# Optimization experiments

Measured on AMD Instinct MI355X. Metric: run time of the kernel, lower is better.

The kernel has to match this reference:

```python
import jax, jax.numpy as jnp
import numpy as np

B, T, D = 2, 2048, 1024
H = 16
HD = D // H  # 64


def _rope_tables(t_len, hd, dtype=jnp.float32):
    inv_freq = 1.0 / (10000.0 ** (jnp.arange(0, hd, 2, dtype=jnp.float32) / hd))
    freqs = jnp.outer(jnp.arange(t_len, dtype=jnp.float32), inv_freq)  # [T, hd/2]
    emb = jnp.concatenate([freqs, freqs], axis=-1)  # [T, hd]
    return emb.astype(dtype)


def _rotate_half(x):
    x1, x2 = jnp.split(x, 2, axis=-1)
    return jnp.concatenate([-x2, x1], axis=-1)


def setup_inputs() -> dict:
    key = jax.random.key(0)
    k1, k2, k3 = jax.random.split(key, 3)
    x = jax.random.normal(k1, (B, T, D), dtype=jnp.float32)
    w_qkv = jax.random.normal(k2, (D, 3 * D), dtype=jnp.float32) * (D ** -0.5)
    w_out = jax.random.normal(k3, (D, D), dtype=jnp.float32) * (D ** -0.5)
    return {"x": x, "w_qkv": w_qkv, "w_out": w_out}


def reference(x, w_qkv, w_out):
    Bc, Tc, Dc = x.shape
    scale = HD ** -0.5
    qkv = x @ w_qkv  # [B,T,3D]
    q, k, v = jnp.split(qkv, 3, axis=-1)
    # -> [B,H,T,hd]
    q = q.reshape(Bc, Tc, H, HD).transpose(0, 2, 1, 3)
    k = k.reshape(Bc, Tc, H, HD).transpose(0, 2, 1, 3)
    v = v.reshape(Bc, Tc, H, HD).transpose(0, 2, 1, 3)
    emb = _rope_tables(Tc, HD, x.dtype)  # [T,hd]
    cos = jnp.cos(emb)[None, None, :, :]
    sin = jnp.sin(emb)[None, None, :, :]
    q = q * cos + _rotate_half(q) * sin
    k = k * cos + _rotate_half(k) * sin
    attn = jnp.einsum('bhqd,bhkd->bhqk', q, k) * scale  # [B,H,T,T]
    causal = jnp.tril(jnp.ones((Tc, Tc), dtype=bool))
    attn = jnp.where(causal[None, None], attn, -jnp.inf)
    attn = jax.nn.softmax(attn, axis=-1)
    out = jnp.einsum('bhqk,bhkd->bhqd', attn, v)
    out = out.transpose(0, 2, 1, 3).reshape(Bc, Tc, Dc)
    return out @ w_out
```

## Files before the change

kernel.cpp:

```cpp
#include <hip/hip_runtime.h>

#define TSEQ 2048
#define DMODEL 1024
#define NHEAD 16
#define HDIM 64
#define NB 2
#define MROWS 4096
#define NQKV 3072
#define QSCALE 0.1803368801111204f
#define ROPE_C (13.2877123795494f / 32.0f)
#define NEGINF -3.0e38f

using s16x8 = __attribute__((ext_vector_type(8))) short;
using s16x4 = __attribute__((ext_vector_type(4))) short;
using f32x4 = __attribute__((ext_vector_type(4))) float;
using u32x2 = __attribute__((ext_vector_type(2))) unsigned int;

static __device__ __forceinline__ float b2f(unsigned short u) {
  union { unsigned int i; float f; } x; x.i = ((unsigned int)u) << 16; return x.f;
}
static __device__ __forceinline__ unsigned short f2b(float f) {
  unsigned int u = __float_as_uint(f);
  u += 0x7fffu + ((u >> 16) & 1u);
  return (unsigned short)(u >> 16);
}

typedef const __attribute__((address_space(1))) char gchar;
typedef __attribute__((address_space(3))) char lchar;
static __device__ __forceinline__ void gload_lds16(const void* g, void* l) {
  __builtin_amdgcn_global_load_lds((gchar*)g, (lchar*)l, 16, 0, 0);
}

__global__ __launch_bounds__(256) void k_prep(const float* __restrict__ x,
                                              short* __restrict__ xb,
                                              const float* __restrict__ wq,
                                              short* __restrict__ wqT,
                                              const float* __restrict__ wo,
                                              short* __restrict__ woT) {
  __shared__ float tile[32][33];
  const int blk = blockIdx.x;
  const int tid = threadIdx.x;
  if (blk < 4096) {
    const int i = blk * 256 + tid;
    const float4 v = ((const float4*)x)[i];
    s16x4 o;
    o.x = (short)f2b(v.x); o.y = (short)f2b(v.y);
    o.z = (short)f2b(v.z); o.w = (short)f2b(v.w);
    ((s16x4*)xb)[i] = o;
    return;
  }
  const float* in; short* out; int C, bx, by;
  if (blk < 7168) {
    const int l = blk - 4096; in = wq; out = wqT; C = NQKV;
    bx = l % 96; by = l / 96;
  } else {
    const int l = blk - 7168; in = wo; out = woT; C = DMODEL;
    bx = l & 31; by = l >> 5;
  }
  const int tx = tid & 31, ty4 = (tid >> 5) * 4;
#pragma unroll
  for (int i = 0; i < 4; ++i)
    tile[ty4 + i][tx] = in[(by * 32 + ty4 + i) * C + bx * 32 + tx];
  __syncthreads();
#pragma unroll
  for (int i = 0; i < 4; ++i)
    out[(bx * 32 + ty4 + i) * DMODEL + by * 32 + tx] = (short)f2b(tile[tx][ty4 + i]);
}

__global__ __launch_bounds__(256) void k_gemm_qkv(const short* __restrict__ A,
                                                  const short* __restrict__ BT,
                                                  short* __restrict__ Qo,
                                                  short* __restrict__ Ko,
                                                  short* __restrict__ Vt) {
  __shared__ __attribute__((aligned(16))) short As[128 * 64];
  __shared__ __attribute__((aligned(16))) short Bs[128 * 64];
  const int K = DMODEL;
  const int tid = threadIdx.x;
  const int wave = tid >> 6, lane = tid & 63, quad = lane >> 4, l15 = lane & 15;
  const int wm = (wave >> 1) * 64, wn = (wave & 1) * 64;
  const int m0 = blockIdx.y * 128, n0 = blockIdx.x * 128;
  f32x4 acc[4][4] = {};
  const char* Ab = (const char*)A;
  const char* Bb = (const char*)BT;
  char* AsB = (char*)As;
  char* BsB = (char*)Bs;
  int srow[4], sg[4];
#pragma unroll
  for (int p = 0; p < 4; ++p) {
    const int i = p * 256 + tid;
    srow[p] = i >> 3;
    sg[p] = (i & 7) ^ (srow[p] & 7);
  }
  for (int k0 = 0; k0 < K; k0 += 64) {
    __syncthreads();
#pragma unroll
    for (int p = 0; p < 4; ++p) {
      const long go = ((long)(m0 + srow[p]) * K + k0) * 2 + sg[p] * 16;
      gload_lds16(Ab + go, AsB + p * 4096 + wave * 1024);
    }
#pragma unroll
    for (int p = 0; p < 4; ++p) {
      const long go = ((long)(n0 + srow[p]) * K + k0) * 2 + sg[p] * 16;
      gload_lds16(Bb + go, BsB + p * 4096 + wave * 1024);
    }
    __syncthreads();
#pragma unroll
    for (int hf = 0; hf < 2; ++hf) {
      s16x8 af[4], bf[4];
#pragma unroll
      for (int i = 0; i < 4; ++i) {
        const int ra = wm + i * 16 + l15;
        af[i] = *(const s16x8*)(AsB + ra * 128 + (((hf * 4 + quad) ^ (ra & 7)) * 16));
        const int rb = wn + i * 16 + l15;
        bf[i] = *(const s16x8*)(BsB + rb * 128 + (((hf * 4 + quad) ^ (rb & 7)) * 16));
      }
#pragma unroll
      for (int i = 0; i < 4; ++i)
#pragma unroll
        for (int j = 0; j < 4; ++j)
          acc[i][j] = __builtin_amdgcn_mfma_f32_16x16x32_bf16(af[i], bf[j], acc[i][j], 0, 0, 0);
    }
  }
  const int colbase = n0 + wn;
  const int region = colbase >> 10;
  const int hh = (colbase & 1023) >> 6;
  const int bq = m0 >> 11;
  const int tbase = (m0 & 2047) + wm;
  if (region == 2) {
    short* dst = Vt + (((long)(bq * NHEAD + hh) * HDIM) << 11);
#pragma unroll
    for (int i = 0; i < 4; ++i) {
      const int t0 = tbase + i * 16 + quad * 4;
#pragma unroll
      for (int j = 0; j < 4; ++j) {
        const int d = j * 16 + l15;
        s16x4 w;
        w.x = (short)f2b(acc[i][j][0]);
        w.y = (short)f2b(acc[i][j][1]);
        w.z = (short)f2b(acc[i][j][2]);
        w.w = (short)f2b(acc[i][j][3]);
        *(s16x4*)(dst + (((long)d) << 11) + t0) = w;
      }
    }
  } else {
    short* dst = (region ? Ko : Qo) + (long)(bq * NHEAD + hh) * TSEQ * HDIM;
#pragma unroll
    for (int i = 0; i < 4; ++i)
#pragma unroll
      for (int j = 0; j < 4; ++j) {
        const int d = j * 16 + l15;
#pragma unroll
        for (int r = 0; r < 4; ++r) {
          const int t = tbase + i * 16 + quad * 4 + r;
          dst[(long)t * HDIM + d] = (short)f2b(acc[i][j][r]);
        }
      }
  }
}

__global__ __launch_bounds__(256) void k_ropek(short* __restrict__ Kp) {
  const int tt = blockIdx.x, bh = blockIdx.y;
  const int tid = threadIdx.x;
  const int row = tid >> 2, chunk = tid & 3;
  const int t = tt * 64 + row;
  short* base = Kp + ((long)bh * TSEQ + t) * HDIM + chunk * 8;
  const s16x8 lo = *(const s16x8*)base;
  const s16x8 hi = *(const s16x8*)(base + 32);
  s16x8 nlo, nhi;
  const float tf = (float)t;
#pragma unroll
  for (int j = 0; j < 8; ++j) {
    const float inv = exp2f(-(float)(chunk * 8 + j) * ROPE_C);
    float sn, cs;
    __sincosf(tf * inv, &sn, &cs);
    const float a = b2f((unsigned short)lo[j]);
    const float b = b2f((unsigned short)hi[j]);
    nlo[j] = (short)f2b(a * cs - b * sn);
    nhi[j] = (short)f2b(b * cs + a * sn);
  }
  *(s16x8*)base = nlo;
  *(s16x8*)(base + 32) = nhi;
}

template <int IM, bool OUT_BF16>
__global__ __launch_bounds__(256) void k_gemm(const short* __restrict__ A,
                                              const short* __restrict__ BT,
                                              void* __restrict__ Cv,
                                              int M, int N, int K) {
  __shared__ __attribute__((aligned(16))) short As[IM * 32 * 64];
  __shared__ __attribute__((aligned(16))) short Bs[128 * 64];
  const int tid = threadIdx.x;
  const int wave = tid >> 6, lane = tid & 63, quad = lane >> 4, l15 = lane & 15;
  const int wm = (wave >> 1) * (IM * 16), wn = (wave & 1) * 64;
  const int m0 = blockIdx.y * (IM * 32), n0 = blockIdx.x * 128;
  f32x4 acc[IM][4] = {};
  const char* Ab = (const char*)A;
  const char* Bb = (const char*)BT;
  char* AsB = (char*)As;
  char* BsB = (char*)Bs;
  int srow[4], sg[4];
#pragma unroll
  for (int p = 0; p < 4; ++p) {
    const int i = p * 256 + tid;
    srow[p] = i >> 3;
    sg[p] = (i & 7) ^ (srow[p] & 7);
  }
  for (int k0 = 0; k0 < K; k0 += 64) {
    __syncthreads();
#pragma unroll
    for (int p = 0; p < IM; ++p) {
      const long go = ((long)(m0 + srow[p]) * K + k0) * 2 + sg[p] * 16;
      gload_lds16(Ab + go, AsB + p * 4096 + wave * 1024);
    }
#pragma unroll
    for (int p = 0; p < 4; ++p) {
      const long go = ((long)(n0 + srow[p]) * K + k0) * 2 + sg[p] * 16;
      gload_lds16(Bb + go, BsB + p * 4096 + wave * 1024);
    }
    __syncthreads();
#pragma unroll
    for (int hf = 0; hf < 2; ++hf) {
      s16x8 af[IM], bf[4];
#pragma unroll
      for (int i = 0; i < IM; ++i) {
        const int ra = wm + i * 16 + l15;
        af[i] = *(const s16x8*)(AsB + ra * 128 + (((hf * 4 + quad) ^ (ra & 7)) * 16));
      }
#pragma unroll
      for (int j = 0; j < 4; ++j) {
        const int rb = wn + j * 16 + l15;
        bf[j] = *(const s16x8*)(BsB + rb * 128 + (((hf * 4 + quad) ^ (rb & 7)) * 16));
      }
#pragma unroll
      for (int i = 0; i < IM; ++i)
#pragma unroll
        for (int j = 0; j < 4; ++j)
          acc[i][j] = __builtin_amdgcn_mfma_f32_16x16x32_bf16(af[i], bf[j], acc[i][j], 0, 0, 0);
    }
  }
#pragma unroll
  for (int i = 0; i < IM; ++i) {
    const int row = m0 + wm + i * 16 + quad * 4;
#pragma unroll
    for (int j = 0; j < 4; ++j) {
      const int col = n0 + wn + j * 16 + l15;
#pragma unroll
      for (int r = 0; r < 4; ++r) {
        if (OUT_BF16) ((short*)Cv)[(long)(row + r) * N + col] = (short)f2b(acc[i][j][r]);
        else          ((float*)Cv)[(long)(row + r) * N + col] = acc[i][j][r];
      }
    }
  }
}

__global__ __launch_bounds__(512) __attribute__((amdgpu_waves_per_eu(4)))
void k_attn(const short* __restrict__ Qg,
            const short* __restrict__ Kg,
            const short* __restrict__ Vg,
            short* __restrict__ O) {
  __shared__ __attribute__((aligned(16))) short Ks[2][64 * 64];
  __shared__ __attribute__((aligned(16))) short Vs[2][64 * 64];
  __shared__ __attribute__((aligned(16))) short pl[8][16 * 64];
  const int bx = blockIdx.x, by = blockIdx.y;
  const int qi = ((by >> 4) & 1) ? (15 - bx) : bx;
  const int bh = by;
  const int b = bh >> 4, h = bh & 15;
  const int tid = threadIdx.x, wave = tid >> 6, lane = tid & 63;
  const int quad = lane >> 4, l15 = lane & 15;
  const char* Kb = (const char*)(Kg + (long)bh * TSEQ * HDIM);
  const char* Vb = (const char*)(Vg + (long)bh * HDIM * TSEQ);
  const short* Qb = Qg + (long)bh * TSEQ * HDIM;
  const int qr0 = qi * 128 + wave * 16;
  const s16x8 rq0 = *(const s16x8*)&Qb[(qr0 + l15) * HDIM + quad * 8];
  const s16x8 rq1 = *(const s16x8*)&Qb[(qr0 + l15) * HDIM + 32 + quad * 8];
  s16x8 aq0, aq1;
  {
    const float tf = (float)(qr0 + l15);
#pragma unroll
    for (int j = 0; j < 8; ++j) {
      const float inv = exp2f(-(float)(quad * 8 + j) * ROPE_C);
      float sn, cs;
      __sincosf(tf * inv, &sn, &cs);
      sn *= QSCALE; cs *= QSCALE;
      const float q0 = b2f((unsigned short)rq0[j]);
      const float q1 = b2f((unsigned short)rq1[j]);
      aq0[j] = (short)f2b(q0 * cs - q1 * sn);
      aq1[j] = (short)f2b(q1 * cs + q0 * sn);
    }
  }
  f32x4 o[4] = {};
  float lsum = 0.0f;
  const int kr0 = tid >> 3, kg0 = (tid & 7) ^ (kr0 & 7);
  char* KsB = (char*)Ks;
  char* VsB = (char*)Vs;
  char* plwB = (char*)pl + wave * 2048;
  const int ldsw = wave * 1024;

#define STAGE(kjv, buf)                                                     \
  do {                                                                      \
    gload_lds16(Kb + (kjv) * 8192 + (kr0 * 8 + kg0) * 16,                   \
                KsB + (buf) * 8192 + ldsw);                                 \
    gload_lds16(Vb + (kjv) * 128 + kr0 * (TSEQ * 2) + kg0 * 16,             \
                VsB + (buf) * 8192 + ldsw);                                 \
  } while (0)

  STAGE(0, 0);
  __syncthreads();

  const int kjmax = 2 * qi + 1;
  const int kjd = qr0 >> 6;
  for (int kj = 0; kj <= kjmax; ++kj) {
    const int cur = kj & 1;
    if (kj < kjmax) STAGE(kj + 1, cur ^ 1);
    if (kj <= kjd) {
      const char* kb = KsB + cur * 8192;
      const char* vb = VsB + cur * 8192;
      f32x4 s[4];
#pragma unroll
      for (int j2 = 0; j2 < 4; ++j2) {
        const int row = j2 * 16 + l15;
        const s16x8 k0 = *(const s16x8*)(kb + row * 128 + ((quad ^ (row & 7)) * 16));
        const s16x8 k1 = *(const s16x8*)(kb + row * 128 + (((4 + quad) ^ (row & 7)) * 16));
        f32x4 z = {};
        z = __builtin_amdgcn_mfma_f32_16x16x32_bf16(k0, aq0, z, 0, 0, 0);
        z = __builtin_amdgcn_mfma_f32_16x16x32_bf16(k1, aq1, z, 0, 0, 0);
        s[j2] = z;
      }
      if (kj == kjd) {
        const int qloc = (qr0 & 63) + l15;
#pragma unroll
        for (int j2 = 0; j2 < 4; ++j2)
#pragma unroll
          for (int r = 0; r < 4; ++r)
            if (j2 * 16 + quad * 4 + r > qloc) s[j2][r] = NEGINF;
      }
      float ps = 0.0f;
#pragma unroll
      for (int j2 = 0; j2 < 4; ++j2) {
        const unsigned int u0 = __float_as_uint(exp2f(s[j2][0])) & 0xffff0000u;
        const unsigned int u1 = __float_as_uint(exp2f(s[j2][1])) & 0xffff0000u;
        const unsigned int u2 = __float_as_uint(exp2f(s[j2][2])) & 0xffff0000u;
        const unsigned int u3 = __float_as_uint(exp2f(s[j2][3])) & 0xffff0000u;
        ps += __uint_as_float(u0) + __uint_as_float(u1) +
              __uint_as_float(u2) + __uint_as_float(u3);
        u32x2 w;
        w.x = (u0 >> 16) | u1;
        w.y = (u2 >> 16) | u3;
        const int t0 = j2 * 16 + quad * 4;
        *(u32x2*)(plwB + l15 * 128 + (((t0 >> 3) ^ (l15 & 7)) * 16) + (quad & 1) * 8) = w;
      }
      lsum += ps;
      const s16x8 bp0 = *(const s16x8*)(plwB + l15 * 128 + ((quad ^ (l15 & 7)) * 16));
      const s16x8 bp1 = *(const s16x8*)(plwB + l15 * 128 + (((4 + quad) ^ (l15 & 7)) * 16));
#pragma unroll
      for (int hs = 0; hs < 4; ++hs) {
        const int d = hs * 16 + l15;
        const s16x8 av0 = *(const s16x8*)(vb + d * 128 + ((quad ^ (d & 7)) * 16));
        const s16x8 av1 = *(const s16x8*)(vb + d * 128 + (((4 + quad) ^ (d & 7)) * 16));
        o[hs] = __builtin_amdgcn_mfma_f32_16x16x32_bf16(av0, bp0, o[hs], 0, 0, 0);
        o[hs] = __builtin_amdgcn_mfma_f32_16x16x32_bf16(av1, bp1, o[hs], 0, 0, 0);
      }
    }
    __syncthreads();
  }
#undef STAGE
  lsum += __shfl_xor(lsum, 16);
  lsum += __shfl_xor(lsum, 32);
  const float rinv = 1.0f / lsum;
  const int t = qr0 + l15;
  short* Orow = O + (long)(b * TSEQ + t) * DMODEL + h * HDIM + quad * 4;
#pragma unroll
  for (int hs = 0; hs < 4; ++hs) {
    s16x4 w;
    w.x = (short)f2b(o[hs][0] * rinv);
    w.y = (short)f2b(o[hs][1] * rinv);
    w.z = (short)f2b(o[hs][2] * rinv);
    w.w = (short)f2b(o[hs][3] * rinv);
    *(s16x4*)(Orow + hs * 16) = w;
  }
}

extern "C" void kernel_launch(void* const* d_in, const int* in_sizes, int n_in,
                              void* d_out, int out_size, void* d_ws, size_t ws_size,
                              hipStream_t stream) {
  const float* x = (const float*)d_in[0];
  const float* w_qkv = (const float*)d_in[1];
  const float* w_out = (const float*)d_in[2];
  float* out = (float*)d_out;
  char* ws = (char*)d_ws;

  short* xb    = (short*)(ws);
  short* wqkvT = (short*)(ws + (8ll << 20));
  short* woutT = (short*)(ws + (14ll << 20));
  short* Qb    = (short*)(ws + (16ll << 20));
  short* Kb    = (short*)(ws + (24ll << 20));
  short* Vt    = (short*)(ws + (32ll << 20));
  short* Ob    = (short*)(ws + (40ll << 20));

  k_prep<<<dim3(8192), dim3(256), 0, stream>>>(x, xb, w_qkv, wqkvT, w_out, woutT);
  k_gemm_qkv<<<dim3(NQKV / 128, MROWS / 128), dim3(256), 0, stream>>>(
      xb, wqkvT, Qb, Kb, Vt);
  k_ropek<<<dim3(TSEQ / 64, NB * NHEAD), dim3(256), 0, stream>>>(Kb);
  k_attn<<<dim3(TSEQ / 128, NB * NHEAD), dim3(512), 0, stream>>>(Qb, Kb, Vt, Ob);
  k_gemm<2, false><<<dim3(DMODEL / 128, MROWS / 64), dim3(256), 0, stream>>>(
      Ob, woutT, (void*)out, MROWS, DMODEL, DMODEL);
}
```

Measured before the change: 193.9 us.

## Fuse K RoPE into QKV GEMM epilogue and tighten attention loop sync

```diff
diff --git a/kernel.cpp b/kernel.cpp
--- a/kernel.cpp
+++ b/kernel.cpp
@@ -24,6 +24,12 @@
   u += 0x7fffu + ((u >> 16) & 1u);
   return (unsigned short)(u >> 16);
 }
+
+#if __has_builtin(__builtin_amdgcn_exp2f)
+#define EXP2(x) __builtin_amdgcn_exp2f(x)
+#else
+#define EXP2(x) exp2f(x)
+#endif
 
 typedef const __attribute__((address_space(1))) char gchar;
 typedef __attribute__((address_space(3))) char lchar;
@@ -143,6 +149,25 @@
       }
     }
   } else {
+    if (region == 1) {
+#pragma unroll
+      for (int i = 0; i < 4; ++i)
+#pragma unroll
+        for (int j = 0; j < 2; ++j) {
+          const int d = j * 16 + l15;
+          const float inv = exp2f(-(float)d * ROPE_C);
+#pragma unroll
+          for (int r = 0; r < 4; ++r) {
+            const int t = tbase + i * 16 + quad * 4 + r;
+            float sn, cs;
+            __sincosf((float)t * inv, &sn, &cs);
+            const float a = acc[i][j][r];
+            const float bv = acc[i][j + 2][r];
+            acc[i][j][r]     = a * cs - bv * sn;
+            acc[i][j + 2][r] = bv * cs + a * sn;
+          }
+        }
+    }
     short* dst = (region ? Ko : Qo) + (long)(bq * NHEAD + hh) * TSEQ * HDIM;
 #pragma unroll
     for (int i = 0; i < 4; ++i)
@@ -156,30 +181,6 @@
         }
       }
   }
-}
-
-__global__ __launch_bounds__(256) void k_ropek(short* __restrict__ Kp) {
-  const int tt = blockIdx.x, bh = blockIdx.y;
-  const int tid = threadIdx.x;
-  const int row = tid >> 2, chunk = tid & 3;
-  const int t = tt * 64 + row;
-  short* base = Kp + ((long)bh * TSEQ + t) * HDIM + chunk * 8;
-  const s16x8 lo = *(const s16x8*)base;
-  const s16x8 hi = *(const s16x8*)(base + 32);
-  s16x8 nlo, nhi;
-  const float tf = (float)t;
-#pragma unroll
-  for (int j = 0; j < 8; ++j) {
-    const float inv = exp2f(-(float)(chunk * 8 + j) * ROPE_C);
-    float sn, cs;
-    __sincosf(tf * inv, &sn, &cs);
-    const float a = b2f((unsigned short)lo[j]);
-    const float b = b2f((unsigned short)hi[j]);
-    nlo[j] = (short)f2b(a * cs - b * sn);
-    nhi[j] = (short)f2b(b * cs + a * sn);
-  }
-  *(s16x8*)base = nlo;
-  *(s16x8*)(base + 32) = nhi;
 }
 
 template <int IM, bool OUT_BF16>
@@ -288,8 +289,11 @@
       aq1[j] = (short)f2b(q1 * cs + q0 * sn);
     }
   }
+  s16x8 ones;
+#pragma unroll
+  for (int j = 0; j < 8; ++j) ones[j] = (short)0x3F80;
   f32x4 o[4] = {};
-  float lsum = 0.0f;
+  f32x4 zs = {};
   const int kr0 = tid >> 3, kg0 = (tid & 7) ^ (kr0 & 7);
   char* KsB = (char*)Ks;
   char* VsB = (char*)Vs;
@@ -305,17 +309,23 @@
   } while (0)
 
   STAGE(0, 0);
-  __syncthreads();
 
   const int kjmax = 2 * qi + 1;
   const int kjd = qr0 >> 6;
   for (int kj = 0; kj <= kjmax; ++kj) {
     const int cur = kj & 1;
-    if (kj < kjmax) STAGE(kj + 1, cur ^ 1);
+    if (kj < kjmax) {
+      STAGE(kj + 1, cur ^ 1);
+      asm volatile("s_waitcnt vmcnt(2)" ::: "memory");
+    } else {
+      asm volatile("s_waitcnt vmcnt(0)" ::: "memory");
+    }
+    __builtin_amdgcn_s_barrier();
     if (kj <= kjd) {
       const char* kb = KsB + cur * 8192;
       const char* vb = VsB + cur * 8192;
       f32x4 s[4];
+      __builtin_amdgcn_s_setprio(1);
 #pragma unroll
       for (int j2 = 0; j2 < 4; ++j2) {
         const int row = j2 * 16 + l15;
@@ -326,6 +336,7 @@
         z = __builtin_amdgcn_mfma_f32_16x16x32_bf16(k1, aq1, z, 0, 0, 0);
         s[j2] = z;
       }
+      __builtin_amdgcn_s_setprio(0);
       if (kj == kjd) {
         const int qloc = (qr0 & 63) + l15;
 #pragma unroll
@@ -334,24 +345,23 @@
           for (int r = 0; r < 4; ++r)
             if (j2 * 16 + quad * 4 + r > qloc) s[j2][r] = NEGINF;
       }
-      float ps = 0.0f;
 #pragma unroll
       for (int j2 = 0; j2 < 4; ++j2) {
-        const unsigned int u0 = __float_as_uint(exp2f(s[j2][0])) & 0xffff0000u;
-        const unsigned int u1 = __float_as_uint(exp2f(s[j2][1])) & 0xffff0000u;
-        const unsigned int u2 = __float_as_uint(exp2f(s[j2][2])) & 0xffff0000u;
-        const unsigned int u3 = __float_as_uint(exp2f(s[j2][3])) & 0xffff0000u;
-        ps += __uint_as_float(u0) + __uint_as_float(u1) +
-              __uint_as_float(u2) + __uint_as_float(u3);
+        const unsigned int u0 = __float_as_uint(EXP2(s[j2][0])) & 0xffff0000u;
+        const unsigned int u1 = __float_as_uint(EXP2(s[j2][1])) & 0xffff0000u;
+        const unsigned int u2 = __float_as_uint(EXP2(s[j2][2])) & 0xffff0000u;
+        const unsigned int u3 = __float_as_uint(EXP2(s[j2][3])) & 0xffff0000u;
         u32x2 w;
         w.x = (u0 >> 16) | u1;
         w.y = (u2 >> 16) | u3;
         const int t0 = j2 * 16 + quad * 4;
         *(u32x2*)(plwB + l15 * 128 + (((t0 >> 3) ^ (l15 & 7)) * 16) + (quad & 1) * 8) = w;
       }
-      lsum += ps;
       const s16x8 bp0 = *(const s16x8*)(plwB + l15 * 128 + ((quad ^ (l15 & 7)) * 16));
       const s16x8 bp1 = *(const s16x8*)(plwB + l15 * 128 + (((4 + quad) ^ (l15 & 7)) * 16));
+      __builtin_amdgcn_s_setprio(1);
+      zs = __builtin_amdgcn_mfma_f32_16x16x32_bf16(ones, bp0, zs, 0, 0, 0);
+      zs = __builtin_amdgcn_mfma_f32_16x16x32_bf16(ones, bp1, zs, 0, 0, 0);
 #pragma unroll
       for (int hs = 0; hs < 4; ++hs) {
         const int d = hs * 16 + l15;
@@ -360,13 +370,13 @@
         o[hs] = __builtin_amdgcn_mfma_f32_16x16x32_bf16(av0, bp0, o[hs], 0, 0, 0);
         o[hs] = __builtin_amdgcn_mfma_f32_16x16x32_bf16(av1, bp1, o[hs], 0, 0, 0);
       }
-    }
-    __syncthreads();
+      __builtin_amdgcn_s_setprio(0);
+    }
+    asm volatile("s_waitcnt lgkmcnt(0)" ::: "memory");
+    __builtin_amdgcn_s_barrier();
   }
 #undef STAGE
-  lsum += __shfl_xor(lsum, 16);
-  lsum += __shfl_xor(lsum, 32);
-  const float rinv = 1.0f / lsum;
+  const float rinv = 1.0f / zs[0];
   const int t = qr0 + l15;
   short* Orow = O + (long)(b * TSEQ + t) * DMODEL + h * HDIM + quad * 4;
 #pragma unroll
@@ -400,7 +410,6 @@
   k_prep<<<dim3(8192), dim3(256), 0, stream>>>(x, xb, w_qkv, wqkvT, w_out, woutT);
   k_gemm_qkv<<<dim3(NQKV / 128, MROWS / 128), dim3(256), 0, stream>>>(
       xb, wqkvT, Qb, Kb, Vt);
-  k_ropek<<<dim3(TSEQ / 64, NB * NHEAD), dim3(256), 0, stream>>>(Kb);
   k_attn<<<dim3(TSEQ / 128, NB * NHEAD), dim3(512), 0, stream>>>(Qb, Kb, Vt, Ob);
   k_gemm<2, false><<<dim3(DMODEL / 128, MROWS / 64), dim3(256), 0, stream>>>(
       Ob, woutT, (void*)out, MROWS, DMODEL, DMODEL);
```

Result: faster. 181.3 us (-6.5%).
